# Performance work log

Hardware: AMD Instinct MI355X
Metric: run time of the kernel (lower is better)

Reference implementation:

```python
import jax, jax.numpy as jnp
import numpy as np

PSP_SIZES = (1, 4, 8, 16)


def conv1x1(x, w, b):
    # x: (b, cin, t, v), w: (cout, cin), b: (cout,)
    return jnp.einsum('bctv,oc->botv', x, w) + b[None, :, None, None]


def psp(feats):
    # Faithful to torch: feats.view(-1, c, t) is a RAW reshape of (n,c,t,v)
    # into (n*v, c, t) (it interleaves t and v); then AdaptiveAvgPool1d over
    # the last axis. With t divisible by every size, adaptive pool == block mean.
    n, c, t, v = feats.shape
    f = feats.reshape(n * v, c, t)
    outs = []
    for s in PSP_SIZES:
        p = f.reshape(n * v, c, s, t // s).mean(axis=-1)  # (n*v, c, s)
        outs.append(p.reshape(n, c, s * v))               # raw reshape, matches torch
    return jnp.concatenate(outs, axis=-1)                 # (n, c, sum(s)*v)


def setup_inputs() -> dict:
    key = jax.random.key(0)
    ks = jax.random.split(key, 8)
    B, C, T, V = 64, 256, 64, 25
    C2 = C // 2
    std = 0.02
    return {
        'x': jax.random.normal(ks[0], (B, C, T, V), dtype=jnp.float32),
        'g_w': jax.random.normal(ks[1], (C2, C), dtype=jnp.float32) * std,
        'g_b': jnp.zeros((C2,), dtype=jnp.float32),
        'theta_w': jax.random.normal(ks[2], (C2, C), dtype=jnp.float32) * std,
        'theta_b': jnp.zeros((C2,), dtype=jnp.float32),
        'W_w': jax.random.normal(ks[3], (C, C2), dtype=jnp.float32) * std,
        'W_b': jnp.zeros((C,), dtype=jnp.float32),
        'bn_gamma': jnp.ones((C,), dtype=jnp.float32),
        'bn_beta': jnp.zeros((C,), dtype=jnp.float32),
        'bn_mean': jnp.zeros((C,), dtype=jnp.float32),
        'bn_var': jnp.ones((C,), dtype=jnp.float32),
    }


def reference(x, g_w, g_b, theta_w, theta_b, W_w, W_b, bn_gamma, bn_beta, bn_mean, bn_var):
    B, C, T, V = x.shape
    C2 = C // 2
    eps = 1e-5

    # g branch: conv1x1 (dropout is identity in eval) -> PSP multi-scale pool
    g_x = psp(conv1x1(x, g_w, g_b))          # (B, C2, S), S = 29*V
    phi = g_x                                 # (B, C2, S)
    g_perm = jnp.swapaxes(g_x, 1, 2)          # (B, S, C2)

    # theta branch
    theta = conv1x1(x, theta_w, theta_b).reshape(B, C2, T * V)
    theta = jnp.swapaxes(theta, 1, 2)         # (B, T*V, C2)

    f = jnp.einsum('bnc,bcs->bns', theta, phi)    # (B, T*V, S)
    f = jax.nn.softmax(f, axis=-2)                # softmax over queries (dim=-2)
    y = jnp.einsum('bns,bsc->bnc', f, g_perm)     # (B, T*V, C2)
    y = jax.nn.softmax(y, axis=-2)                # softmax over T*V again

    y = jnp.swapaxes(y, 1, 2).reshape(B, C2, T, V)
    y = conv1x1(y, W_w, W_b)                      # (B, C, T, V)

    z = y + x
    inv = jax.lax.rsqrt(bn_var + eps)
    z = (z - bn_mean[None, :, None, None]) * (inv * bn_gamma)[None, :, None, None] + bn_beta[None, :, None, None]
    return jax.nn.relu(z)
```

## Files before the change

### kernel.cpp

```cpp
#include <hip/hip_runtime.h>

#define NTB 25

typedef float f32x4 __attribute__((ext_vector_type(4)));
typedef short bf16x8 __attribute__((ext_vector_type(8)));

__device__ __forceinline__ ushort f2bf(float f) {
    union { float f; uint u; } v; v.f = f;
    uint u = v.u;
    return (ushort)((u + 0x7fffu + ((u >> 16) & 1u)) >> 16);
}
__device__ __forceinline__ float bf2f(ushort h) {
    union { uint u; float f; } v; v.u = ((uint)h) << 16;
    return v.f;
}
__device__ __forceinline__ int foff(int p, int k32) {
    return (((p & 15) | (((k32 >> 3) & 3) << 4)) << 3) + (k32 & 7);
}

__global__ __launch_bounds__(256) void k0_wconv(
    const float* __restrict__ gw, const float* __restrict__ tw,
    const float* __restrict__ Ww,
    ushort* __restrict__ gwb, ushort* __restrict__ twb, ushort* __restrict__ Wbf)
{
    int idx = blockIdx.x * 256 + threadIdx.x;
    if (idx < 8192) {
        const float* src = (idx < 4096) ? gw : tw;
        ushort* dst = (idx < 4096) ? gwb : twb;
        int u = idx & 4095;
        int o = u >> 5, c0 = (u & 31) << 3;
        ushort* d = dst + ((o >> 4) * 8 + (c0 >> 5)) * 512 + foff(o, c0 & 31);
        #pragma unroll
        for (int j = 0; j < 8; ++j) d[j] = f2bf(src[o * 256 + c0 + j]);
    } else if (idx < 12288) {
        int u = idx - 8192;
        int o = u >> 4, c0 = (u & 15) << 3;
        ushort* d = Wbf + ((o >> 4) * 4 + (c0 >> 5)) * 512 + foff(o, c0 & 31);
        #pragma unroll
        for (int j = 0; j < 8; ++j) d[j] = f2bf(Ww[o * 128 + c0 + j]);
    }
}

__global__ __launch_bounds__(256) void k1a_xpose(const float* __restrict__ x,
                                                 ushort* __restrict__ xT)
{
    int blk = blockIdx.x;
    int nt = blk % NTB; blk /= NTB;
    int cb = blk & 3; int b = blk >> 2;
    int n0 = nt * 64, c0 = cb * 64;
    __shared__ ushort lds[64 * 70];
    int tid = threadIdx.x;

    const float* xb = x + ((size_t)b * 256 + c0) * 1600 + n0;
    #pragma unroll
    for (int p = 0; p < 4; ++p) {
        int idx = tid + p * 256;
        int c = idx >> 4, n4 = idx & 15;
        float4 v = *reinterpret_cast<const float4*>(&xb[(size_t)c * 1600 + n4 * 4]);
        ushort4 pk;
        pk.x = f2bf(v.x); pk.y = f2bf(v.y); pk.z = f2bf(v.z); pk.w = f2bf(v.w);
        *reinterpret_cast<ushort4*>(&lds[c * 70 + n4 * 4]) = pk;
    }
    __syncthreads();
    #pragma unroll
    for (int q = 0; q < 2; ++q) {
        int t2 = tid + q * 256;
        int nl = t2 >> 3, c8 = t2 & 7;
        int n = n0 + nl, c = c0 + c8 * 8;
        bf16x8 r;
        #pragma unroll
        for (int j = 0; j < 8; ++j)
            r[j] = (short)lds[(c8 * 8 + j) * 70 + nl];
        *reinterpret_cast<bf16x8*>(
            &xT[(size_t)b * 409600 + (size_t)((n >> 4) * 8 + (c >> 5)) * 512 +
                foff(n, c & 31)]) = r;
    }
}

__global__ __launch_bounds__(256) void k1b_conv(
    const ushort* __restrict__ xT,
    const ushort* __restrict__ gwb, const float* __restrict__ gb,
    const ushort* __restrict__ twb, const float* __restrict__ tb,
    ushort* __restrict__ gout, ushort* __restrict__ thT)
{
    int nt = blockIdx.x % NTB, b = blockIdx.x / NTB;
    int n0 = nt * 64;
    int tid = threadIdx.x, lane = tid & 63, w = tid >> 6;
    int lr = lane & 15, lg = lane >> 4;
    const ushort* xb = xT + (size_t)b * 409600;

    if (w < 2) {
        int o0 = w * 64;
        f32x4 acc[4][4] = {};
        #pragma unroll
        for (int kc = 0; kc < 8; ++kc) {
            bf16x8 a[4], bf[4];
            #pragma unroll
            for (int mi = 0; mi < 4; ++mi)
                a[mi] = *reinterpret_cast<const bf16x8*>(
                    &xb[(size_t)(((n0 >> 4) + mi) * 8 + kc) * 512 + lane * 8]);
            #pragma unroll
            for (int ni = 0; ni < 4; ++ni)
                bf[ni] = *reinterpret_cast<const bf16x8*>(
                    &gwb[(size_t)(((o0 >> 4) + ni) * 8 + kc) * 512 + lane * 8]);
            #pragma unroll
            for (int mi = 0; mi < 4; ++mi)
                #pragma unroll
                for (int ni = 0; ni < 4; ++ni)
                    acc[mi][ni] = __builtin_amdgcn_mfma_f32_16x16x32_bf16(
                        a[mi], bf[ni], acc[mi][ni], 0, 0, 0);
        }
        #pragma unroll
        for (int ni = 0; ni < 4; ++ni) {
            int o = o0 + ni * 16 + lr;
            float bs = gb[o];
            ushort* gp = &gout[((size_t)b * 128 + o) * 1600 + n0];
            #pragma unroll
            for (int mi = 0; mi < 4; ++mi) {
                ushort4 pk;
                pk.x = f2bf(acc[mi][ni][0] + bs);
                pk.y = f2bf(acc[mi][ni][1] + bs);
                pk.z = f2bf(acc[mi][ni][2] + bs);
                pk.w = f2bf(acc[mi][ni][3] + bs);
                *reinterpret_cast<ushort4*>(&gp[mi * 16 + lg * 4]) = pk;
            }
        }
    } else {
        int o0 = (w - 2) * 64;
        f32x4 acc[4][4] = {};
        #pragma unroll
        for (int kc = 0; kc < 8; ++kc) {
            bf16x8 a[4], bf[4];
            #pragma unroll
            for (int mi = 0; mi < 4; ++mi)
                a[mi] = *reinterpret_cast<const bf16x8*>(
                    &twb[(size_t)(((o0 >> 4) + mi) * 8 + kc) * 512 + lane * 8]);
            #pragma unroll
            for (int ni = 0; ni < 4; ++ni)
                bf[ni] = *reinterpret_cast<const bf16x8*>(
                    &xb[(size_t)(((n0 >> 4) + ni) * 8 + kc) * 512 + lane * 8]);
            #pragma unroll
            for (int mi = 0; mi < 4; ++mi)
                #pragma unroll
                for (int ni = 0; ni < 4; ++ni)
                    acc[mi][ni] = __builtin_amdgcn_mfma_f32_16x16x32_bf16(
                        a[mi], bf[ni], acc[mi][ni], 0, 0, 0);
        }
        #pragma unroll
        for (int mi = 0; mi < 4; ++mi) {
            float4 tbv = *reinterpret_cast<const float4*>(&tb[o0 + mi * 16 + lg * 4]);
            float tbb[4] = {tbv.x, tbv.y, tbv.z, tbv.w};
            int cq = o0 + mi * 16 + lg * 4;
            #pragma unroll
            for (int ni = 0; ni < 4; ++ni) {
                int n = n0 + ni * 16 + lr;
                ushort4 pk;
                pk.x = f2bf(acc[mi][ni][0] + tbb[0]);
                pk.y = f2bf(acc[mi][ni][1] + tbb[1]);
                pk.z = f2bf(acc[mi][ni][2] + tbb[2]);
                pk.w = f2bf(acc[mi][ni][3] + tbb[3]);
                *reinterpret_cast<ushort4*>(
                    &thT[(size_t)b * 204800 + (size_t)((n >> 4) * 4 + (cq >> 5)) * 512 +
                         foff(n, cq & 31)]) = pk;
            }
        }
    }
}

__global__ __launch_bounds__(256) void k2a_psp(const ushort* __restrict__ g,
                                               ushort* __restrict__ phiC,
                                               ushort* __restrict__ phiT)
{
    int cc = blockIdx.x & 7, b = blockIdx.x >> 3;
    __shared__ ushort pooled[16][776];
    int tid = threadIdx.x;

    #pragma unroll
    for (int it = 0; it < 2; ++it) {
        int item = tid + it * 256;
        if (item < 400) {
            int cl = item / 25, r = item % 25;
            const ushort* gp = g + ((size_t)((b * 128 + cc * 16 + cl) * 25 + r)) * 64;
            float S4[16];
            #pragma unroll
            for (int q = 0; q < 8; ++q) {
                bf16x8 v = *reinterpret_cast<const bf16x8*>(&gp[q * 8]);
                S4[q * 2]     = bf2f((ushort)v[0]) + bf2f((ushort)v[1]) +
                                bf2f((ushort)v[2]) + bf2f((ushort)v[3]);
                S4[q * 2 + 1] = bf2f((ushort)v[4]) + bf2f((ushort)v[5]) +
                                bf2f((ushort)v[6]) + bf2f((ushort)v[7]);
            }
            float S8[8], S16[4];
            float tot = 0.f;
            #pragma unroll
            for (int k = 0; k < 8; ++k) S8[k] = S4[2 * k] + S4[2 * k + 1];
            #pragma unroll
            for (int k = 0; k < 4; ++k) { S16[k] = S8[2 * k] + S8[2 * k + 1]; tot += S16[k]; }
            ushort* row = pooled[cl];
            row[r] = f2bf(tot * (1.f / 64.f));
            #pragma unroll
            for (int k = 0; k < 4; ++k)  row[25 + 4 * r + k]  = f2bf(S16[k] * 0.0625f);
            #pragma unroll
            for (int k = 0; k < 8; ++k)  row[125 + 8 * r + k] = f2bf(S8[k] * 0.125f);
            #pragma unroll
            for (int k = 0; k < 16; ++k) row[325 + 16 * r + k] = f2bf(S4[k] * 0.25f);
        }
    }
    if (tid < 16) {
        ushort* row = pooled[tid];
        for (int j = 725; j < 768; ++j) row[j] = 0;
    }
    __syncthreads();

    {
        ushort* pc = phiC + (size_t)(b * 128 + cc * 16) * 768;
        #pragma unroll
        for (int i = 0; i < 6; ++i) {
            int q = tid + i * 256;
            int cl = q / 96, j8 = (q % 96) * 8;
            bf16x8 v = *reinterpret_cast<const bf16x8*>(&pooled[cl][j8]);
            *reinterpret_cast<bf16x8*>(&pc[(size_t)cl * 768 + j8]) = v;
        }
    }
    {
        ushort* pt = phiT + (size_t)b * 98304 + (size_t)(cc >> 1) * 512 + (cc & 1) * 256;
        #pragma unroll
        for (int i = 0; i < 6; ++i) {
            int slot = tid + i * 256;
            int jt = slot >> 5, lh = slot & 31;
            int jl = jt * 16 + (lh & 15);
            int cb8 = (lh >> 4) * 8;
            bf16x8 v;
            #pragma unroll
            for (int jj = 0; jj < 8; ++jj)
                v[jj] = (short)pooled[cb8 + jj][jl];
            *reinterpret_cast<bf16x8*>(&pt[(size_t)(jt * 4) * 512 + lh * 8]) = v;
        }
    }
}

__global__ __launch_bounds__(256) void k3_expf(
    const ushort* __restrict__ thT, const ushort* __restrict__ phiT,
    ushort* __restrict__ E, float* __restrict__ psum, int b0)
{
    int blk = blockIdx.x;
    int st = blk % 12; blk /= 12;
    int nt = blk % 25; int bl = blk / 25;
    int b = b0 + bl;
    int n0 = nt * 64, s0 = st * 64;
    int tid = threadIdx.x, lane = tid & 63, w = tid >> 6;
    int lr = lane & 15, lg = lane >> 4;

    __shared__ ushort Bs[8192];
    __shared__ float red[64][4];

    {
        const ushort* src = phiT + (size_t)b * 98304 + (size_t)(s0 >> 4) * 2048;
        #pragma unroll
        for (int t = 0; t < 4; ++t) {
            int o8 = (t * 256 + tid) * 8;
            *reinterpret_cast<bf16x8*>(&Bs[o8]) =
                *reinterpret_cast<const bf16x8*>(&src[o8]);
        }
    }
    bf16x8 A[4];
    #pragma unroll
    for (int kc = 0; kc < 4; ++kc)
        A[kc] = *reinterpret_cast<const bf16x8*>(
            &thT[(size_t)b * 204800 + (size_t)(((n0 >> 4) + w) * 4 + kc) * 512 + lane * 8]);
    __syncthreads();

    f32x4 acc[4] = {};
    #pragma unroll
    for (int kc = 0; kc < 4; ++kc)
        #pragma unroll
        for (int ni = 0; ni < 4; ++ni) {
            bf16x8 bb = *reinterpret_cast<const bf16x8*>(&Bs[(ni * 4 + kc) * 512 + lane * 8]);
            acc[ni] = __builtin_amdgcn_mfma_f32_16x16x32_bf16(A[kc], bb, acc[ni], 0, 0, 0);
        }

    size_t ebase = (size_t)bl * 1228800 + (size_t)(((n0 >> 4) + w) * 24 + (s0 >> 5)) * 512;
    #pragma unroll
    for (int ni = 0; ni < 4; ++ni) {
        float se = 0.f;
        float ex[4];
        #pragma unroll
        for (int r = 0; r < 4; ++r) { ex[r] = __expf(acc[ni][r]); se += ex[r]; }
        int scadd = (ni >> 1) * 512;
        int khi = ((ni & 1) * 2 + (lr >> 3)) & 3;
        #pragma unroll
        for (int r = 0; r < 4; ++r) {
            int p = lg * 4 + r;
            E[ebase + scadd + ((p | (khi << 4)) << 3) + (lr & 7)] = f2bf(ex[r]);
        }
        se += __shfl_xor(se, 16);
        se += __shfl_xor(se, 32);
        if (lg == 0) red[ni * 16 + lr][w] = se;
    }
    __syncthreads();
    if (tid < 64) {
        float z = red[tid][0] + red[tid][1] + red[tid][2] + red[tid][3];
        psum[((size_t)b * 768 + s0 + tid) * 25 + nt] = z;
    }
}

__global__ __launch_bounds__(256) void k4a_zinv(const float* __restrict__ psum,
                                                float* __restrict__ zinv)
{
    int idx = blockIdx.x * 256 + threadIdx.x;
    if (idx >= 32 * 768) return;
    int s = idx % 768;
    const float* p = psum + (size_t)idx * 25;
    float z = 0.f;
    #pragma unroll
    for (int i = 0; i < 25; ++i) z += p[i];
    zinv[idx] = (s < 725) ? 1.f / z : 0.f;
}

__global__ __launch_bounds__(256) void k4b_scale(const ushort* __restrict__ phiC,
                                                 const float* __restrict__ zinv,
                                                 ushort* __restrict__ phiZ)
{
    int idx = blockIdx.x * 256 + threadIdx.x;
    int l = idx & 63;
    int t = idx >> 6;
    int bi = t % 192, b = t / 192;
    int c = (bi / 24) * 16 + (l & 15);
    int s0 = (bi % 24) * 32 + (l >> 4) * 8;
    bf16x8 v = *reinterpret_cast<const bf16x8*>(&phiC[((size_t)b * 128 + c) * 768 + s0]);
    float4 z0 = *reinterpret_cast<const float4*>(&zinv[b * 768 + s0]);
    float4 z1 = *reinterpret_cast<const float4*>(&zinv[b * 768 + s0 + 4]);
    float zz[8] = {z0.x, z0.y, z0.z, z0.w, z1.x, z1.y, z1.z, z1.w};
    bf16x8 r;
    #pragma unroll
    for (int j = 0; j < 8; ++j) r[j] = (short)f2bf(bf2f((ushort)v[j]) * zz[j]);
    *reinterpret_cast<bf16x8*>(&phiZ[(size_t)b * 98304 + (size_t)bi * 512 + l * 8]) = r;
}

__global__ __launch_bounds__(64, 2) void k5_pv(
    const ushort* __restrict__ E, const ushort* __restrict__ phiZ,
    ushort* __restrict__ y, float* __restrict__ ypz, int b0)
{
    int ng = blockIdx.x % 100, bl = blockIdx.x / 100;
    int b = b0 + bl;
    int nrow = ng * 16;
    int lane = threadIdx.x;
    int lr = lane & 15, lg = lane >> 4;
    const ushort* Eb = E + (size_t)bl * 1228800 + (size_t)ng * 24 * 512 + lane * 8;
    const ushort* Pb = phiZ + (size_t)b * 98304 + lane * 8;

    f32x4 acc[8] = {};
    bf16x8 Ab[3], Bb[3][8];
    #pragma unroll
    for (int p = 0; p < 3; ++p) {
        Ab[p] = *reinterpret_cast<const bf16x8*>(&Eb[(size_t)p * 512]);
        #pragma unroll
        for (int cf = 0; cf < 8; ++cf)
            Bb[p][cf] = *reinterpret_cast<const bf16x8*>(&Pb[(size_t)(cf * 24 + p) * 512]);
    }
    #pragma unroll
    for (int kc = 0; kc < 24; ++kc) {
        int cur = kc % 3;
        bf16x8 a = Ab[cur];
        #pragma unroll
        for (int cf = 0; cf < 8; ++cf)
            acc[cf] = __builtin_amdgcn_mfma_f32_16x16x32_bf16(a, Bb[cur][cf], acc[cf], 0, 0, 0);
        if (kc + 3 < 24) {
            Ab[cur] = *reinterpret_cast<const bf16x8*>(&Eb[(size_t)(kc + 3) * 512]);
            #pragma unroll
            for (int cf = 0; cf < 8; ++cf)
                Bb[cur][cf] = *reinterpret_cast<const bf16x8*>(
                    &Pb[(size_t)(cf * 24 + kc + 3) * 512]);
        }
    }

    #pragma unroll
    for (int cf = 0; cf < 8; ++cf) {
        float se = 0.f;
        #pragma unroll
        for (int r = 0; r < 4; ++r) {
            ushort hv = f2bf(acc[cf][r]);
            y[((size_t)b * 1600 + nrow + lg * 4 + r) * 128 + cf * 16 + lr] = hv;
            se += __expf(bf2f(hv));
        }
        se += __shfl_xor(se, 16);
        se += __shfl_xor(se, 32);
        if (lane < 16)
            ypz[((size_t)b * 128 + cf * 16 + lane) * 100 + ng] = se;
    }
}

__global__ void k6b_ycomb(const float* __restrict__ ypz, float* __restrict__ yzi)
{
    int idx = blockIdx.x * 256 + threadIdx.x;
    if (idx >= 64 * 128) return;
    const float* p = ypz + (size_t)idx * 100;
    float z = 0.f;
    for (int i = 0; i < 100; ++i) z += p[i];
    yzi[idx] = 1.f / z;
}

__global__ __launch_bounds__(256) void k7_final(
    const ushort* __restrict__ y, const float* __restrict__ yzi,
    const ushort* __restrict__ Wbf, const float* __restrict__ Wb,
    const float* __restrict__ x,
    const float* __restrict__ gamma, const float* __restrict__ beta,
    const float* __restrict__ mean, const float* __restrict__ var,
    float* __restrict__ out)
{
    int nt = blockIdx.x % NTB, b = blockIdx.x / NTB;
    int n0 = nt * 64;
    __shared__ ushort yl[64][136];
    __shared__ float scl[256], shl[256], wbl[256], zl[128];
    int t = threadIdx.x, lane = t & 63, w = t >> 6;
    {
        float sc = gamma[t] * rsqrtf(var[t] + 1e-5f);
        scl[t] = sc;
        shl[t] = beta[t] - mean[t] * sc;
        wbl[t] = Wb[t];
        if (t < 128) zl[t] = yzi[(size_t)b * 128 + t];
    }
    __syncthreads();
    int c8 = (t & 15) * 8, rr = t >> 4;
    #pragma unroll
    for (int p = 0; p < 4; ++p) {
        int r = rr + 16 * p;
        bf16x8 v = *reinterpret_cast<const bf16x8*>(
            &y[((size_t)b * 1600 + n0 + r) * 128 + c8]);
        bf16x8 pk;
        #pragma unroll
        for (int j = 0; j < 8; ++j) {
            float f = bf2f((ushort)v[j]);
            pk[j] = (short)f2bf(__expf(f) * zl[c8 + j]);
        }
        *reinterpret_cast<bf16x8*>(&yl[r][c8]) = pk;
    }
    __syncthreads();
    int lr = lane & 15, lg = lane >> 4;
    int o0 = w * 64;
    f32x4 acc[4][4] = {};
    #pragma unroll
    for (int kc = 0; kc < 4; ++kc) {
        bf16x8 af[4];
        #pragma unroll
        for (int mi = 0; mi < 4; ++mi)
            af[mi] = *reinterpret_cast<const bf16x8*>(
                &Wbf[(size_t)(((o0 >> 4) + mi) * 4 + kc) * 512 + lane * 8]);
        #pragma unroll
        for (int ni = 0; ni < 4; ++ni) {
            bf16x8 bfrag = *reinterpret_cast<const bf16x8*>(&yl[ni * 16 + lr][kc * 32 + lg * 8]);
            #pragma unroll
            for (int mi = 0; mi < 4; ++mi)
                acc[mi][ni] = __builtin_amdgcn_mfma_f32_16x16x32_bf16(
                    af[mi], bfrag, acc[mi][ni], 0, 0, 0);
        }
    }
    #pragma unroll
    for (int mi = 0; mi < 4; ++mi)
        #pragma unroll
        for (int ni = 0; ni < 4; ++ni) {
            int n = n0 + ni * 16 + lr;
            #pragma unroll
            for (int r = 0; r < 4; ++r) {
                int o = o0 + mi * 16 + lg * 4 + r;
                size_t off = ((size_t)b * 256 + o) * 1600 + n;
                float v = (acc[mi][ni][r] + wbl[o] + x[off]) * scl[o] + shl[o];
                out[off] = fmaxf(v, 0.f);
            }
        }
}

extern "C" void kernel_launch(void* const* d_in, const int* in_sizes, int n_in,
                              void* d_out, int out_size, void* d_ws, size_t ws_size,
                              hipStream_t stream)
{
    const float* x   = (const float*)d_in[0];
    const float* gw  = (const float*)d_in[1];
    const float* gb  = (const float*)d_in[2];
    const float* tw  = (const float*)d_in[3];
    const float* tb  = (const float*)d_in[4];
    const float* Ww  = (const float*)d_in[5];
    const float* Wb  = (const float*)d_in[6];
    const float* bng = (const float*)d_in[7];
    const float* bnb = (const float*)d_in[8];
    const float* bnm = (const float*)d_in[9];
    const float* bnv = (const float*)d_in[10];
    float* out = (float*)d_out;

    char* base = (char*)d_ws;
    ushort* thT  = (ushort*)(base);
    ushort* gout = (ushort*)(base + 26214400);
    ushort* phiC = (ushort*)(base + 52428800);
    ushort* phiT = (ushort*)(base + 65011712);
    float* psum  = (float*)(base + 77594624);
    ushort* phiZ = (ushort*)(base + 82509824);
    float* zinv  = (float*)(base + 95092736);
    float* ypz   = (float*)(base + 95289344);
    float* yzi   = (float*)(base + 98566144);
    ushort* Wbf  = (ushort*)(base + 98598912);
    ushort* gwb  = (ushort*)(base + 98664448);
    ushort* twb  = (ushort*)(base + 98729984);
    ushort* yv   = gout;
    ushort* xT   = (ushort*)d_out;
    ushort* E    = (ushort*)d_out;

    k0_wconv<<<48, 256, 0, stream>>>(gw, tw, Ww, gwb, twb, Wbf);
    k1a_xpose<<<64 * 4 * NTB, 256, 0, stream>>>(x, xT);
    k1b_conv<<<64 * NTB, 256, 0, stream>>>(xT, gwb, gb, twb, tb, gout, thT);
    k2a_psp<<<64 * 8, 256, 0, stream>>>(gout, phiC, phiT);

    k3_expf<<<32 * 25 * 12, 256, 0, stream>>>(thT, phiT, E, psum, 0);
    k4a_zinv<<<96, 256, 0, stream>>>(psum, zinv);
    k4b_scale<<<1536, 256, 0, stream>>>(phiC, zinv, phiZ);
    k5_pv<<<32 * 100, 64, 0, stream>>>(E, phiZ, yv, ypz, 0);

    k3_expf<<<32 * 25 * 12, 256, 0, stream>>>(thT, phiT, E, psum, 32);
    k4a_zinv<<<96, 256, 0, stream>>>(psum + (size_t)32 * 768 * 25, zinv);
    k4b_scale<<<1536, 256, 0, stream>>>(phiC + (size_t)32 * 128 * 768, zinv,
                                        phiZ + (size_t)32 * 98304);
    k5_pv<<<32 * 100, 64, 0, stream>>>(E, phiZ, yv, ypz, 32);

    k6b_ycomb<<<32, 256, 0, stream>>>(ypz, yzi);
    k7_final<<<64 * NTB, 256, 0, stream>>>(yv, yzi, Wbf, Wb, x, bng, bnb, bnm, bnv, out);
}
```

Measured before the change: 306.0 us.

## Compute two row tiles per PV wave and transpose partial-sum layouts for coalescing

Measured after the change: 311.1 us. About the same (+1.7%).

```diff
diff --git a/kernel.cpp b/kernel.cpp
--- a/kernel.cpp
+++ b/kernel.cpp
@@ -300,20 +300,20 @@
     __syncthreads();
     if (tid < 64) {
         float z = red[tid][0] + red[tid][1] + red[tid][2] + red[tid][3];
-        psum[((size_t)b * 768 + s0 + tid) * 25 + nt] = z;
+        psum[(size_t)nt * 49152 + (size_t)b * 768 + s0 + tid] = z;
     }
 }
 
 __global__ __launch_bounds__(256) void k4a_zinv(const float* __restrict__ psum,
-                                                float* __restrict__ zinv)
+                                                float* __restrict__ zinv, int b0)
 {
     int idx = blockIdx.x * 256 + threadIdx.x;
     if (idx >= 32 * 768) return;
-    int s = idx % 768;
-    const float* p = psum + (size_t)idx * 25;
+    int s = idx % 768, bh = idx / 768;
+    size_t base = (size_t)(b0 + bh) * 768 + s;
     float z = 0.f;
     #pragma unroll
-    for (int i = 0; i < 25; ++i) z += p[i];
+    for (int i = 0; i < 25; ++i) z += psum[(size_t)i * 49152 + base];
     zinv[idx] = (s < 725) ? 1.f / z : 0.f;
 }
 
@@ -341,19 +341,19 @@
     const ushort* __restrict__ E, const ushort* __restrict__ phiZ,
     ushort* __restrict__ y, float* __restrict__ ypz, int b0)
 {
-    int ng = blockIdx.x % 100, bl = blockIdx.x / 100;
+    int ng2 = blockIdx.x % 50, bl = blockIdx.x / 50;
     int b = b0 + bl;
-    int nrow = ng * 16;
     int lane = threadIdx.x;
     int lr = lane & 15, lg = lane >> 4;
-    const ushort* Eb = E + (size_t)bl * 1228800 + (size_t)ng * 24 * 512 + lane * 8;
+    const ushort* Eb = E + (size_t)bl * 1228800 + (size_t)(ng2 * 2) * 24 * 512 + lane * 8;
     const ushort* Pb = phiZ + (size_t)b * 98304 + lane * 8;
 
-    f32x4 acc[8] = {};
-    bf16x8 Ab[3], Bb[3][8];
+    f32x4 acc[2][8] = {};
+    bf16x8 Ab[3][2], Bb[3][8];
     #pragma unroll
     for (int p = 0; p < 3; ++p) {
-        Ab[p] = *reinterpret_cast<const bf16x8*>(&Eb[(size_t)p * 512]);
+        Ab[p][0] = *reinterpret_cast<const bf16x8*>(&Eb[(size_t)p * 512]);
+        Ab[p][1] = *reinterpret_cast<const bf16x8*>(&Eb[(size_t)(24 + p) * 512]);
         #pragma unroll
         for (int cf = 0; cf < 8; ++cf)
             Bb[p][cf] = *reinterpret_cast<const bf16x8*>(&Pb[(size_t)(cf * 24 + p) * 512]);
@@ -361,12 +361,16 @@
     #pragma unroll
     for (int kc = 0; kc < 24; ++kc) {
         int cur = kc % 3;
-        bf16x8 a = Ab[cur];
-        #pragma unroll
-        for (int cf = 0; cf < 8; ++cf)
-            acc[cf] = __builtin_amdgcn_mfma_f32_16x16x32_bf16(a, Bb[cur][cf], acc[cf], 0, 0, 0);
+        bf16x8 a0 = Ab[cur][0], a1 = Ab[cur][1];
+        #pragma unroll
+        for (int cf = 0; cf < 8; ++cf) {
+            bf16x8 bbv = Bb[cur][cf];
+            acc[0][cf] = __builtin_amdgcn_mfma_f32_16x16x32_bf16(a0, bbv, acc[0][cf], 0, 0, 0);
+            acc[1][cf] = __builtin_amdgcn_mfma_f32_16x16x32_bf16(a1, bbv, acc[1][cf], 0, 0, 0);
+        }
         if (kc + 3 < 24) {
-            Ab[cur] = *reinterpret_cast<const bf16x8*>(&Eb[(size_t)(kc + 3) * 512]);
+            Ab[cur][0] = *reinterpret_cast<const bf16x8*>(&Eb[(size_t)(kc + 3) * 512]);
+            Ab[cur][1] = *reinterpret_cast<const bf16x8*>(&Eb[(size_t)(24 + kc + 3) * 512]);
             #pragma unroll
             for (int cf = 0; cf < 8; ++cf)
                 Bb[cur][cf] = *reinterpret_cast<const bf16x8*>(
@@ -375,18 +379,23 @@
     }
 
     #pragma unroll
-    for (int cf = 0; cf < 8; ++cf) {
-        float se = 0.f;
-        #pragma unroll
-        for (int r = 0; r < 4; ++r) {
-            ushort hv = f2bf(acc[cf][r]);
-            y[((size_t)b * 1600 + nrow + lg * 4 + r) * 128 + cf * 16 + lr] = hv;
-            se += __expf(bf2f(hv));
-        }
-        se += __shfl_xor(se, 16);
-        se += __shfl_xor(se, 32);
-        if (lane < 16)
-            ypz[((size_t)b * 128 + cf * 16 + lane) * 100 + ng] = se;
+    for (int m = 0; m < 2; ++m) {
+        int ng = ng2 * 2 + m;
+        int nrow = ng * 16;
+        #pragma unroll
+        for (int cf = 0; cf < 8; ++cf) {
+            float se = 0.f;
+            #pragma unroll
+            for (int r = 0; r < 4; ++r) {
+                ushort hv = f2bf(acc[m][cf][r]);
+                y[((size_t)b * 1600 + nrow + lg * 4 + r) * 128 + cf * 16 + lr] = hv;
+                se += __expf(bf2f(hv));
+            }
+            se += __shfl_xor(se, 16);
+            se += __shfl_xor(se, 32);
+            if (lane < 16)
+                ypz[((size_t)ng * 64 + b) * 128 + cf * 16 + lane] = se;
+        }
     }
 }
 
@@ -394,9 +403,8 @@
 {
     int idx = blockIdx.x * 256 + threadIdx.x;
     if (idx >= 64 * 128) return;
-    const float* p = ypz + (size_t)idx * 100;
     float z = 0.f;
-    for (int i = 0; i < 100; ++i) z += p[i];
+    for (int ng = 0; ng < 100; ++ng) z += ypz[(size_t)ng * 8192 + idx];
     yzi[idx] = 1.f / z;
 }
 
@@ -510,15 +518,15 @@
     k2a_psp<<<64 * 8, 256, 0, stream>>>(gout, phiC, phiT);
 
     k3_expf<<<32 * 25 * 12, 256, 0, stream>>>(thT, phiT, E, psum, 0);
-    k4a_zinv<<<96, 256, 0, stream>>>(psum, zinv);
+    k4a_zinv<<<96, 256, 0, stream>>>(psum, zinv, 0);
     k4b_scale<<<1536, 256, 0, stream>>>(phiC, zinv, phiZ);
-    k5_pv<<<32 * 100, 64, 0, stream>>>(E, phiZ, yv, ypz, 0);
+    k5_pv<<<32 * 50, 64, 0, stream>>>(E, phiZ, yv, ypz, 0);
 
     k3_expf<<<32 * 25 * 12, 256, 0, stream>>>(thT, phiT, E, psum, 32);
-    k4a_zinv<<<96, 256, 0, stream>>>(psum + (size_t)32 * 768 * 25, zinv);
+    k4a_zinv<<<96, 256, 0, stream>>>(psum, zinv, 32);
     k4b_scale<<<1536, 256, 0, stream>>>(phiC + (size_t)32 * 128 * 768, zinv,
                                         phiZ + (size_t)32 * 98304);
-    k5_pv<<<32 * 100, 64, 0, stream>>>(E, phiZ, yv, ypz, 32);
+    k5_pv<<<32 * 50, 64, 0, stream>>>(E, phiZ, yv, ypz, 32);
 
     k6b_ycomb<<<32, 256, 0, stream>>>(ypz, yzi);
     k7_final<<<64 * NTB, 256, 0, stream>>>(yv, yzi, Wbf, Wb, x, bng, bnb, bnm, bnv, out);
```
